# Kernel tuning notes

Hardware: AMD Instinct MI355X
Metric: run time of the kernel (lower is better)

The kernel has to match this reference:

```python
import jax, jax.numpy as jnp
import numpy as np

B, S, T = 4, 512, 512
V, D, F, H, DK, N = 32000, 512, 2048, 8, 64, 6
PAD = 0

# sinusoidal positional encoding table, matching the torch source exactly
_pos = np.arange(max(S, T))[:, None]
_i = np.arange(D // 2)[None, :]
_ang = _pos / (10000.0 ** (2 * _i / D))
_pe = np.empty((max(S, T), D), dtype=np.float32)
_pe[:, 0::2] = np.sin(_ang)
_pe[:, 1::2] = np.cos(_ang)
PE = jnp.asarray(_pe)


def setup_inputs() -> dict:
    key = jax.random.key(0)
    ks = iter(jax.random.split(key, 64))
    s = 0.02
    w = lambda shape: jax.random.normal(next(ks), shape, jnp.float32) * s
    inp = {
        'src': jax.random.randint(next(ks), (B, S), 0, V, jnp.int32),
        'trg': jax.random.randint(next(ks), (B, T), 0, V, jnp.int32),
        'emb_src': w((V, D)).at[PAD].set(0.0),
        'emb_trg': w((V, D)).at[PAD].set(0.0),
        # encoder stacks (leading axis = layer)
        'enc_wq': w((N, D, H * DK)), 'enc_wk': w((N, D, H * DK)),
        'enc_wv': w((N, D, H * DK)), 'enc_wo': w((N, H * DK, D)),
        'enc_ln1_g': jnp.ones((N, D)), 'enc_ln1_b': jnp.zeros((N, D)),
        'enc_w1': w((N, D, F)), 'enc_b1': jnp.zeros((N, F)),
        'enc_w2': w((N, F, D)), 'enc_b2': jnp.zeros((N, D)),
        'enc_ln2_g': jnp.ones((N, D)), 'enc_ln2_b': jnp.zeros((N, D)),
        # decoder stacks
        'dec_wq': w((N, D, H * DK)), 'dec_wk': w((N, D, H * DK)),
        'dec_wv': w((N, D, H * DK)), 'dec_wo': w((N, H * DK, D)),
        'dec_ln1_g': jnp.ones((N, D)), 'dec_ln1_b': jnp.zeros((N, D)),
        'dec_cq': w((N, D, H * DK)), 'dec_ck': w((N, D, H * DK)),
        'dec_cv': w((N, D, H * DK)), 'dec_co': w((N, H * DK, D)),
        'dec_ln2_g': jnp.ones((N, D)), 'dec_ln2_b': jnp.zeros((N, D)),
        'dec_w1': w((N, D, F)), 'dec_b1': jnp.zeros((N, F)),
        'dec_w2': w((N, F, D)), 'dec_b2': jnp.zeros((N, D)),
        'dec_ln3_g': jnp.ones((N, D)), 'dec_ln3_b': jnp.zeros((N, D)),
        'proj': w((D, V)),
    }
    return inp


def _ln(x, g, b, eps=1e-5):
    m = x.mean(-1, keepdims=True)
    v = ((x - m) ** 2).mean(-1, keepdims=True)
    return (x - m) * jax.lax.rsqrt(v + eps) * g + b


def _mha(xq, xkv, wq, wk, wv, wo, mask):
    b, lq, _ = xq.shape
    lk = xkv.shape[1]
    q = (xq @ wq).reshape(b, lq, H, DK).transpose(0, 2, 1, 3)   # bhqd
    k = (xkv @ wk).reshape(b, lk, H, DK).transpose(0, 2, 1, 3)  # bhkd
    v = (xkv @ wv).reshape(b, lk, H, DK).transpose(0, 2, 1, 3)  # bhkd
    scores = jnp.einsum('bhqd,bhkd->bhqk', q, k)
    scores = jnp.where(mask, -jnp.inf, scores)
    attn = jax.nn.softmax(scores * (DK ** -0.5), axis=-1)
    out = jnp.einsum('bhqk,bhkd->bhqd', attn, v)
    out = out.transpose(0, 2, 1, 3).reshape(b, lq, H * DK)
    return out @ wo


def _ffn(x, w1, b1, w2, b2):
    return jax.nn.relu(x @ w1 + b1) @ w2 + b2


def reference(src, trg, emb_src, emb_trg,
              enc_wq, enc_wk, enc_wv, enc_wo, enc_ln1_g, enc_ln1_b,
              enc_w1, enc_b1, enc_w2, enc_b2, enc_ln2_g, enc_ln2_b,
              dec_wq, dec_wk, dec_wv, dec_wo, dec_ln1_g, dec_ln1_b,
              dec_cq, dec_ck, dec_cv, dec_co, dec_ln2_g, dec_ln2_b,
              dec_w1, dec_b1, dec_w2, dec_b2, dec_ln3_g, dec_ln3_b,
              proj):
    scale = D ** 0.5
    src_pad = (src == PAD)[:, None, None, :]                 # [B,1,1,S]
    trg_pad = (trg == PAD)[:, None, None, :]                 # [B,1,1,T]
    causal = jnp.triu(jnp.ones((T, T), bool), 1)[None, None]  # [1,1,T,T]
    trg_mask = trg_pad | causal

    # encoder (dropout = identity in eval)
    x = emb_src[src] * scale + PE[None, :S]

    def enc_step(h, p):
        wq, wk, wv, wo, g1, b1, w1, bb1, w2, bb2, g2, b2 = p
        h = _ln(h + _mha(h, h, wq, wk, wv, wo, src_pad), g1, b1)
        h = _ln(h + _ffn(h, w1, bb1, w2, bb2), g2, b2)
        return h, None

    x_enc, _ = jax.lax.scan(enc_step, x,
        (enc_wq, enc_wk, enc_wv, enc_wo, enc_ln1_g, enc_ln1_b,
         enc_w1, enc_b1, enc_w2, enc_b2, enc_ln2_g, enc_ln2_b))

    # decoder
    y = emb_trg[trg] * scale + PE[None, :T]

    def dec_step(h, p):
        (wq, wk, wv, wo, g1, b1, cq, ck, cv, co, g2, b2,
         w1, bb1, w2, bb2, g3, b3) = p
        h = _ln(h + _mha(h, h, wq, wk, wv, wo, trg_mask), g1, b1)
        h = _ln(h + _mha(h, x_enc, cq, ck, cv, co, src_pad), g2, b2)
        h = _ln(h + _ffn(h, w1, bb1, w2, bb2), g3, b3)
        return h, None

    y, _ = jax.lax.scan(dec_step, y,
        (dec_wq, dec_wk, dec_wv, dec_wo, dec_ln1_g, dec_ln1_b,
         dec_cq, dec_ck, dec_cv, dec_co, dec_ln2_g, dec_ln2_b,
         dec_w1, dec_b1, dec_w2, dec_b2, dec_ln3_g, dec_ln3_b))

    return y @ proj  # [B, T, trg_vocab]
```

## Files before the change

kernel.cpp:

```cpp
#include <hip/hip_runtime.h>
#include <math.h>

#define BBATCH 4
#define SS 512
#define DDIM 512
#define FFN 2048
#define NHEAD 8
#define DHEAD 64
#define NL 6
#define NVOC 32000
#define MTOK (BBATCH*SS)
#define PAD_ID 0
#define MSZE ((size_t)MTOK * DDIM)

typedef unsigned short u16;
typedef __attribute__((ext_vector_type(8))) short short8;
typedef __attribute__((ext_vector_type(4))) float f32x4;

__device__ __forceinline__ u16 f2bf(float f) {
    union { float f; unsigned u; } v; v.f = f;
    unsigned r = ((v.u >> 16) & 1u) + 0x7fffu;
    return (u16)((v.u + r) >> 16);
}

__device__ __forceinline__ void gload16(const u16* g, u16* l) {
    __builtin_amdgcn_global_load_lds(
        (const __attribute__((address_space(1))) void*)g,
        (__attribute__((address_space(3))) void*)l, 16, 0, 0);
}

template<int N> __device__ __forceinline__ void waitv() {
    if constexpr (N == 0)      asm volatile("s_waitcnt vmcnt(0)" ::: "memory");
    else if constexpr (N == 2) asm volatile("s_waitcnt vmcnt(2)" ::: "memory");
    else if constexpr (N == 3) asm volatile("s_waitcnt vmcnt(3)" ::: "memory");
    else if constexpr (N == 4) asm volatile("s_waitcnt vmcnt(4)" ::: "memory");
    else if constexpr (N == 6) asm volatile("s_waitcnt vmcnt(6)" ::: "memory");
    else if constexpr (N == 8) asm volatile("s_waitcnt vmcnt(8)" ::: "memory");
    __builtin_amdgcn_sched_barrier(0);
}
__device__ __forceinline__ void rawbar() {
    __builtin_amdgcn_s_barrier();
    __builtin_amdgcn_sched_barrier(0);
}

template<int BM, int BN, int OUTBF, int RELU, int BIAS>
__device__ __forceinline__ void gemm_core(
    u16* __restrict__ AsB, u16* __restrict__ BsB,
    const u16* __restrict__ A, int lda,
    const u16* __restrict__ B, int ldb,
    void* __restrict__ Cv, int ldc,
    int row0, int col0, int K, const float* __restrict__ bias)
{
    const int tid  = threadIdx.x;
    const int lane = tid & 63;
    const int wid  = tid >> 6;
    const int wr   = wid >> 1, wc = wid & 1;
    constexpr int MF = BM / 32, NF = BN / 32, RA = BM / 64, RB = BN / 64;
    constexpr int LPT = RA + RB;

    const u16* aSrc[RA]; int aOff[RA];
    #pragma unroll
    for (int r = 0; r < RA; r++) {
        int row = (tid >> 2) + r * 64;
        int slot = ((tid & 3) << 4) ^ ((row & 3) << 4);
        aSrc[r] = A + (size_t)(row0 + row) * lda + (slot >> 1);
        aOff[r] = r * 2048 + tid * 8;
    }
    const u16* bSrc[RB]; int bOff[RB];
    #pragma unroll
    for (int r = 0; r < RB; r++) {
        int row = (tid >> 2) + r * 64;
        int slot = ((tid & 3) << 4) ^ ((row & 3) << 4);
        bSrc[r] = B + (size_t)(col0 + row) * ldb + (slot >> 1);
        bOff[r] = r * 2048 + tid * 8;
    }

    f32x4 acc[MF][NF];
    const f32x4 zero = {0.f, 0.f, 0.f, 0.f};
    #pragma unroll
    for (int m = 0; m < MF; m++)
        #pragma unroll
        for (int n = 0; n < NF; n++) acc[m][n] = zero;

    auto issue = [&](int t) {
        u16* ad = AsB + (t & 3) * (BM * 32);
        u16* bd = BsB + (t & 3) * (BN * 32);
        #pragma unroll
        for (int r = 0; r < RA; r++) gload16(aSrc[r] + t * 32, ad + aOff[r]);
        #pragma unroll
        for (int r = 0; r < RB; r++) gload16(bSrc[r] + t * 32, bd + bOff[r]);
    };
    auto comp = [&](int t) {
        const u16* as = AsB + (t & 3) * (BM * 32);
        const u16* bs = BsB + (t & 3) * (BN * 32);
        short8 af[MF], bf[NF];
        #pragma unroll
        for (int m = 0; m < MF; m++) {
            int row = wr * (BM / 2) + m * 16 + (lane & 15);
            int slot = ((lane >> 4) << 4) ^ ((row & 3) << 4);
            af[m] = *(const short8*)&as[row * 32 + (slot >> 1)];
        }
        #pragma unroll
        for (int n = 0; n < NF; n++) {
            int row = wc * (BN / 2) + n * 16 + (lane & 15);
            int slot = ((lane >> 4) << 4) ^ ((row & 3) << 4);
            bf[n] = *(const short8*)&bs[row * 32 + (slot >> 1)];
        }
        __builtin_amdgcn_s_setprio(1);
        #pragma unroll
        for (int m = 0; m < MF; m++)
            #pragma unroll
            for (int n = 0; n < NF; n++)
                acc[m][n] = __builtin_amdgcn_mfma_f32_16x16x32_bf16(af[m], bf[n], acc[m][n], 0, 0, 0);
        __builtin_amdgcn_s_setprio(0);
    };

    const int nt = K / 32;
    issue(0); issue(1); issue(2);
    int t = 0;
    for (; t < nt - 2; ++t) {
        waitv<2 * LPT>();
        rawbar();
        if (t + 3 < nt) issue(t + 3);
        comp(t);
    }
    waitv<LPT>(); rawbar(); comp(nt - 2);
    waitv<0>();   rawbar(); comp(nt - 1);

    const int crow = row0 + wr * (BM / 2);
    const int ccol = col0 + wc * (BN / 2);
    #pragma unroll
    for (int m = 0; m < MF; m++) {
        #pragma unroll
        for (int n = 0; n < NF; n++) {
            int col = ccol + n * 16 + (lane & 15);
            float bv = BIAS ? bias[col] : 0.0f;
            #pragma unroll
            for (int i = 0; i < 4; i++) {
                int row = crow + m * 16 + ((lane >> 4) << 2) + i;
                float v = acc[m][n][i] + bv;
                if (RELU) v = fmaxf(v, 0.0f);
                if (OUTBF) ((u16*)Cv)[(size_t)row * ldc + col] = f2bf(v);
                else       ((float*)Cv)[(size_t)row * ldc + col] = v;
            }
        }
    }
}

template<int BM, int BN, int OUTBF, int RELU, int BIAS, int SWZ = 0>
__global__ __launch_bounds__(256) void mgemm(
    const u16* __restrict__ A, int lda, size_t aSb, size_t aSh,
    const u16* __restrict__ B, int ldb, size_t bSb, size_t bSh,
    void* __restrict__ Cv, int ldc, size_t cSb, size_t cSh,
    int K, const float* __restrict__ bias)
{
    __shared__ __align__(16) u16 As[4 * BM * 32];
    __shared__ __align__(16) u16 Bs[4 * BN * 32];
    int bx = blockIdx.x, by = blockIdx.y;
    if (SWZ) {
        int nwg = gridDim.x * gridDim.y;
        int lin = by * gridDim.x + bx;
        int cpx = nwg >> 3;
        int s = (lin & 7) * cpx + (lin >> 3);
        bx = s % gridDim.x; by = s / gridDim.x;
    }
    const int zb = blockIdx.z >> 3, zh = blockIdx.z & 7;
    const u16* Ab = A + (size_t)zb * aSb + (size_t)zh * aSh;
    const u16* Bb = B + (size_t)zb * bSb + (size_t)zh * bSh;
    void* Cb = OUTBF ? (void*)((u16*)Cv + (size_t)zb * cSb + (size_t)zh * cSh)
                     : (void*)((float*)Cv + (size_t)zb * cSb + (size_t)zh * cSh);
    gemm_core<BM, BN, OUTBF, RELU, BIAS>(As, Bs, Ab, lda, Bb, ldb, Cb, ldc,
                                          by * BM, bx * BN, K, bias);
}

template<int BM, int BN>
__global__ __launch_bounds__(256) void mgemm_dual(
    const u16* __restrict__ A1, int lda1, const u16* __restrict__ B1, int ldb1,
    u16* __restrict__ C1, int ldc1, int nx1, int nblk1,
    const u16* __restrict__ A2, int lda2, const u16* __restrict__ B2, int ldb2,
    u16* __restrict__ C2, int ldc2, int nx2,
    int K)
{
    __shared__ __align__(16) u16 As[4 * BM * 32];
    __shared__ __align__(16) u16 Bs[4 * BN * 32];
    int id = blockIdx.x;
    if (id < nblk1) {
        gemm_core<BM, BN, 1, 0, 0>(As, Bs, A1, lda1, B1, ldb1, C1, ldc1,
                                    (id / nx1) * BM, (id % nx1) * BN, K, nullptr);
    } else {
        id -= nblk1;
        gemm_core<BM, BN, 1, 0, 0>(As, Bs, A2, lda2, B2, ldb2, C2, ldc2,
                                    (id / nx2) * BM, (id % nx2) * BN, K, nullptr);
    }
}

template<int CAUSAL>
__global__ __launch_bounds__(512) void flash_attn(
    const u16* __restrict__ Qp, int ldq,
    const u16* __restrict__ Kp, int ldk,
    const u16* __restrict__ Vtp,
    u16* __restrict__ O,
    const int* __restrict__ ids)
{
    __shared__ __align__(16) u16 Kl[3][64 * 64];
    __shared__ __align__(16) u16 Vl[3][64 * 64];
    __shared__ __align__(16) u16 Pl[8][16 * 64];
    __shared__ float msk[SS];

    const int tid = threadIdx.x, lane = tid & 63, wid = tid >> 6;
    const int bh = blockIdx.y, b = bh >> 3, h = bh & 7;
    const int q0 = blockIdx.x * 128;

    for (int i = tid; i < SS; i += 512)
        msk[i] = (ids[b * SS + i] == PAD_ID) ? -1e30f : 0.0f;

    const int qloc = wid * 16 + (lane & 15);
    const u16* Qb = Qp + (size_t)(b * SS + q0 + qloc) * ldq + h * 64 + ((lane >> 4) * 8);
    short8 qf[2];
    qf[0] = *(const short8*)(Qb);
    qf[1] = *(const short8*)(Qb + 32);

    const u16* Kb = Kp + (size_t)b * SS * ldk + h * 64;
    const u16* Vb = Vtp + (size_t)(h * 64) * MTOK + b * SS;

    auto stage = [&](int buf, int kt) {
        int row = tid >> 3;
        int sl  = tid & 7;
        int ls = sl ^ (row & 7);
        gload16(Kb + (size_t)(kt * 64 + row) * ldk + ls * 8, &Kl[buf][row * 64 + sl * 8]);
        gload16(Vb + (size_t)row * MTOK + kt * 64 + ls * 8, &Vl[buf][row * 64 + sl * 8]);
    };

    const int nt = CAUSAL ? (2 * blockIdx.x + 2) : (SS / 64);

    float m_i[4], l_i[4];
    f32x4 o_acc[4];
    const f32x4 zero = {0.f, 0.f, 0.f, 0.f};
    #pragma unroll
    for (int i = 0; i < 4; i++) { m_i[i] = -1e30f; l_i[i] = 0.0f; }
    #pragma unroll
    for (int n = 0; n < 4; n++) o_acc[n] = zero;

    auto comp = [&](int kt) {
        const int cur = kt % 3;
        f32x4 s_acc[4];
        #pragma unroll
        for (int n = 0; n < 4; n++) s_acc[n] = zero;
        __builtin_amdgcn_s_setprio(1);
        #pragma unroll
        for (int kk = 0; kk < 2; kk++) {
            #pragma unroll
            for (int n = 0; n < 4; n++) {
                int row = n * 16 + (lane & 15);
                int ls = (kk * 4 + (lane >> 4)) ^ (row & 7);
                short8 kf = *(const short8*)&Kl[cur][row * 64 + ls * 8];
                s_acc[n] = __builtin_amdgcn_mfma_f32_16x16x32_bf16(qf[kk], kf, s_acc[n], 0, 0, 0);
            }
        }
        __builtin_amdgcn_s_setprio(0);

        float sv[4][4];
        #pragma unroll
        for (int n = 0; n < 4; n++) {
            int kg = kt * 64 + n * 16 + (lane & 15);
            float mk = msk[kg];
            #pragma unroll
            for (int i = 0; i < 4; i++) {
                float s = s_acc[n][i] * 0.125f + mk;
                if (CAUSAL) {
                    int qg = q0 + wid * 16 + ((lane >> 4) << 2) + i;
                    if (kg > qg) s = -1e30f;
                }
                sv[n][i] = s;
            }
        }
        float pm[4], mn[4], rs[4], ps[4];
        #pragma unroll
        for (int i = 0; i < 4; i++)
            pm[i] = fmaxf(fmaxf(sv[0][i], sv[1][i]), fmaxf(sv[2][i], sv[3][i]));
        #pragma unroll
        for (int i = 0; i < 4; i++) {
            #pragma unroll
            for (int msh = 1; msh <= 8; msh <<= 1)
                pm[i] = fmaxf(pm[i], __shfl_xor(pm[i], msh));
            mn[i] = fmaxf(m_i[i], pm[i]);
            rs[i] = __expf(m_i[i] - mn[i]);
            m_i[i] = mn[i];
        }
        float p[4][4];
        #pragma unroll
        for (int n = 0; n < 4; n++)
            #pragma unroll
            for (int i = 0; i < 4; i++)
                p[n][i] = (sv[n][i] < -1e29f) ? 0.0f : __expf(sv[n][i] - mn[i]);
        #pragma unroll
        for (int i = 0; i < 4; i++) {
            ps[i] = p[0][i] + p[1][i] + p[2][i] + p[3][i];
            #pragma unroll
            for (int msh = 1; msh <= 8; msh <<= 1)
                ps[i] += __shfl_xor(ps[i], msh);
            l_i[i] = l_i[i] * rs[i] + ps[i];
        }
        #pragma unroll
        for (int n = 0; n < 4; n++)
            #pragma unroll
            for (int i = 0; i < 4; i++)
                o_acc[n][i] *= rs[i];

        #pragma unroll
        for (int n = 0; n < 4; n++) {
            int k = n * 16 + (lane & 15);
            #pragma unroll
            for (int i = 0; i < 4; i++) {
                int q = ((lane >> 4) << 2) + i;
                Pl[wid][q * 64 + (((k >> 3) ^ (q & 7)) << 3) + (k & 7)] = f2bf(p[n][i]);
            }
        }
        asm volatile("s_waitcnt lgkmcnt(0)" ::: "memory");
        __builtin_amdgcn_sched_barrier(0);

        __builtin_amdgcn_s_setprio(1);
        #pragma unroll
        for (int kk = 0; kk < 2; kk++) {
            int qrow = lane & 15;
            int lsp = (kk * 4 + (lane >> 4)) ^ (qrow & 7);
            short8 pa = *(const short8*)&Pl[wid][qrow * 64 + lsp * 8];
            #pragma unroll
            for (int nf = 0; nf < 4; nf++) {
                int row = nf * 16 + (lane & 15);
                int vs = (kk * 4 + (lane >> 4)) ^ (row & 7);
                short8 vf = *(const short8*)&Vl[cur][row * 64 + vs * 8];
                o_acc[nf] = __builtin_amdgcn_mfma_f32_16x16x32_bf16(pa, vf, o_acc[nf], 0, 0, 0);
            }
        }
        __builtin_amdgcn_s_setprio(0);
    };

    stage(0, 0);
    stage(1, 1);
    int t = 0;
    for (; t < nt - 1; ++t) {
        waitv<2>();
        rawbar();
        if (t + 2 < nt) stage((t + 2) % 3, t + 2);
        comp(t);
    }
    waitv<0>(); rawbar(); comp(nt - 1);

    #pragma unroll
    for (int nf = 0; nf < 4; nf++) {
        int d = h * 64 + nf * 16 + (lane & 15);
        #pragma unroll
        for (int i = 0; i < 4; i++) {
            int qg = b * SS + q0 + wid * 16 + ((lane >> 4) << 2) + i;
            O[(size_t)qg * DDIM + d] = f2bf(o_acc[nf][i] / l_i[i]);
        }
    }
}

__device__ __forceinline__ void transp_core(const float* __restrict__ src, u16* __restrict__ dst,
                                            int N, int K, int n0, int k0)
{
    __shared__ u16 t[64][65];
    const int tid = threadIdx.x;
    #pragma unroll
    for (int i = 0; i < 16; i++) {
        int idx = tid + i * 256;
        int kr = idx >> 6, nc = idx & 63;
        t[kr][nc] = f2bf(src[(size_t)(k0 + kr) * N + n0 + nc]);
    }
    __syncthreads();
    #pragma unroll
    for (int i = 0; i < 16; i++) {
        int idx = tid + i * 256;
        int nr = idx >> 6, kc = idx & 63;
        dst[(size_t)(n0 + nr) * K + k0 + kc] = t[kc][nr];
    }
}

__global__ __launch_bounds__(256) void transp(const float* __restrict__ src, u16* __restrict__ dst,
                                              int N, int K, size_t sStride, size_t dStride)
{
    transp_core(src + (size_t)blockIdx.z * sStride, dst + (size_t)blockIdx.z * dStride,
                N, K, blockIdx.x * 64, blockIdx.y * 64);
}

#define OFF_QK 0u
#define OFF_WV 524288u
#define OFF_WO 786432u
#define OFF_CQ 1048576u
#define OFF_CK 1310720u
#define OFF_CV 1572864u
#define OFF_CO 1835008u
#define OFF_W1 2097152u
#define OFF_W2 3145728u
#define WBLK   4194304u
#define M2CNT  262144u
#define MF1CNT 1048576u

__global__ __launch_bounds__(256) void transpW(
    const float* p0, const float* p1, const float* p2, const float* p3,
    const float* p4, const float* p5, const float* p6, const float* p7,
    const float* p8, const float* p9, const float* p10, const float* p11,
    u16* __restrict__ wreg)
{
    int z = blockIdx.z;
    int w = z % 12, l = z / 12;
    const float* ptrs[12] = {p0,p1,p2,p3,p4,p5,p6,p7,p8,p9,p10,p11};
    const float* src = ptrs[w] + (size_t)l * M2CNT;
    u16* dst = wreg + (w < 4 ? (size_t)l * WBLK + (size_t)w * M2CNT
                             : (size_t)(NL + l) * WBLK + (size_t)(w - 4) * M2CNT);
    transp_core(src, dst, 512, 512, blockIdx.x * 64, blockIdx.y * 64);
}

__global__ __launch_bounds__(256) void transpF1(const float* __restrict__ e,
                                                const float* __restrict__ d, u16* __restrict__ wreg)
{
    int z = blockIdx.z; int l = z % NL, w = z / NL;
    const float* src = (w ? d : e) + (size_t)l * MF1CNT;
    u16* dst = wreg + (size_t)(w * NL + l) * WBLK + OFF_W1;
    transp_core(src, dst, 2048, 512, blockIdx.x * 64, blockIdx.y * 64);
}

__global__ __launch_bounds__(256) void transpF2(const float* __restrict__ e,
                                                const float* __restrict__ d, u16* __restrict__ wreg)
{
    int z = blockIdx.z; int l = z % NL, w = z / NL;
    const float* src = (w ? d : e) + (size_t)l * MF1CNT;
    u16* dst = wreg + (size_t)(w * NL + l) * WBLK + OFF_W2;
    transp_core(src, dst, 512, 2048, blockIdx.x * 64, blockIdx.y * 64);
}

__global__ void pe_kernel(float* __restrict__ PEt)
{
    int pos = blockIdx.x, d = threadIdx.x;
    int i = d >> 1;
    double freq = exp(-(2.0 * (double)i / (double)DDIM) * log(10000.0));
    double ang = (double)pos * freq;
    PEt[pos * DDIM + d] = (float)((d & 1) ? cos(ang) : sin(ang));
}

__global__ void embed_kernel(const int* __restrict__ src, const int* __restrict__ trg,
                             const float* __restrict__ es, const float* __restrict__ et,
                             const float* __restrict__ PEt,
                             float* __restrict__ X, u16* __restrict__ Xb,
                             float* __restrict__ Y, u16* __restrict__ Ybf)
{
    int gtok = blockIdx.x;
    int d = threadIdx.x;
    bool dec = gtok >= MTOK;
    int tok = dec ? gtok - MTOK : gtok;
    int pos = tok & (SS - 1);
    int id = (dec ? trg : src)[tok];
    const float* emb = dec ? et : es;
    float val = emb[(size_t)id * DDIM + d] * 22.62741699796952f + PEt[pos * DDIM + d];
    (dec ? Y : X)[(size_t)tok * DDIM + d] = val;
    (dec ? Ybf : Xb)[(size_t)tok * DDIM + d] = f2bf(val);
}

__global__ __launch_bounds__(256) void add_ln_kernel(float* __restrict__ x,
    const float* __restrict__ addv, const float* __restrict__ g,
    const float* __restrict__ bta, u16* __restrict__ xb)
{
    int row = blockIdx.x;
    int tid = threadIdx.x;
    size_t base = (size_t)row * DDIM;
    __shared__ float sbuf[4];

    float v0 = x[base + tid]       + addv[base + tid];
    float v1 = x[base + tid + 256] + addv[base + tid + 256];

    float s = v0 + v1;
    #pragma unroll
    for (int o = 32; o > 0; o >>= 1) s += __shfl_down(s, o);
    if ((tid & 63) == 0) sbuf[tid >> 6] = s;
    __syncthreads();
    float mean = (sbuf[0] + sbuf[1] + sbuf[2] + sbuf[3]) * (1.0f / DDIM);
    __syncthreads();

    float d0 = v0 - mean, d1 = v1 - mean;
    float ss = d0 * d0 + d1 * d1;
    #pragma unroll
    for (int o = 32; o > 0; o >>= 1) ss += __shfl_down(ss, o);
    if ((tid & 63) == 0) sbuf[tid >> 6] = ss;
    __syncthreads();
    float var = (sbuf[0] + sbuf[1] + sbuf[2] + sbuf[3]) * (1.0f / DDIM);
    float inv = rsqrtf(var + 1e-5f);

    float o0 = d0 * inv * g[tid]       + bta[tid];
    float o1 = d1 * inv * g[tid + 256] + bta[tid + 256];
    x[base + tid] = o0;
    x[base + tid + 256] = o1;
    xb[base + tid] = f2bf(o0);
    xb[base + tid + 256] = f2bf(o1);
}

__global__ __launch_bounds__(256) void add_ln_red(float* __restrict__ x,
    const float* __restrict__ part, const float* __restrict__ bias,
    const float* __restrict__ g, const float* __restrict__ bta, u16* __restrict__ xb)
{
    int row = blockIdx.x;
    int tid = threadIdx.x;
    size_t base = (size_t)row * DDIM;
    __shared__ float sbuf[4];

    float v0 = x[base + tid]       + bias[tid];
    float v1 = x[base + tid + 256] + bias[tid + 256];
    #pragma unroll
    for (int s4 = 0; s4 < 4; s4++) {
        v0 += part[s4 * MSZE + base + tid];
        v1 += part[s4 * MSZE + base + tid + 256];
    }

    float s = v0 + v1;
    #pragma unroll
    for (int o = 32; o > 0; o >>= 1) s += __shfl_down(s, o);
    if ((tid & 63) == 0) sbuf[tid >> 6] = s;
    __syncthreads();
    float mean = (sbuf[0] + sbuf[1] + sbuf[2] + sbuf[3]) * (1.0f / DDIM);
    __syncthreads();

    float d0 = v0 - mean, d1 = v1 - mean;
    float ss = d0 * d0 + d1 * d1;
    #pragma unroll
    for (int o = 32; o > 0; o >>= 1) ss += __shfl_down(ss, o);
    if ((tid & 63) == 0) sbuf[tid >> 6] = ss;
    __syncthreads();
    float var = (sbuf[0] + sbuf[1] + sbuf[2] + sbuf[3]) * (1.0f / DDIM);
    float inv = rsqrtf(var + 1e-5f);

    float o0 = d0 * inv * g[tid]       + bta[tid];
    float o1 = d1 * inv * g[tid + 256] + bta[tid + 256];
    x[base + tid] = o0;
    x[base + tid + 256] = o1;
    xb[base + tid] = f2bf(o0);
    xb[base + tid + 256] = f2bf(o1);
}

extern "C" void kernel_launch(void* const* d_in, const int* in_sizes, int n_in,
                              void* d_out, int out_size, void* d_ws, size_t ws_size,
                              hipStream_t stream)
{
    (void)in_sizes; (void)n_in; (void)out_size;

    const int*   src      = (const int*)  d_in[0];
    const int*   trg      = (const int*)  d_in[1];
    const float* emb_src  = (const float*)d_in[2];
    const float* emb_trg  = (const float*)d_in[3];
    const float* enc_wq   = (const float*)d_in[4];
    const float* enc_wk   = (const float*)d_in[5];
    const float* enc_wv   = (const float*)d_in[6];
    const float* enc_wo   = (const float*)d_in[7];
    const float* enc_ln1g = (const float*)d_in[8];
    const float* enc_ln1b = (const float*)d_in[9];
    const float* enc_w1   = (const float*)d_in[10];
    const float* enc_b1   = (const float*)d_in[11];
    const float* enc_w2   = (const float*)d_in[12];
    const float* enc_b2   = (const float*)d_in[13];
    const float* enc_ln2g = (const float*)d_in[14];
    const float* enc_ln2b = (const float*)d_in[15];
    const float* dec_wq   = (const float*)d_in[16];
    const float* dec_wk   = (const float*)d_in[17];
    const float* dec_wv   = (const float*)d_in[18];
    const float* dec_wo   = (const float*)d_in[19];
    const float* dec_ln1g = (const float*)d_in[20];
    const float* dec_ln1b = (const float*)d_in[21];
    const float* dec_cq   = (const float*)d_in[22];
    const float* dec_ck   = (const float*)d_in[23];
    const float* dec_cv   = (const float*)d_in[24];
    const float* dec_co   = (const float*)d_in[25];
    const float* dec_ln2g = (const float*)d_in[26];
    const float* dec_ln2b = (const float*)d_in[27];
    const float* dec_w1   = (const float*)d_in[28];
    const float* dec_b1   = (const float*)d_in[29];
    const float* dec_w2   = (const float*)d_in[30];
    const float* dec_b2   = (const float*)d_in[31];
    const float* dec_ln3g = (const float*)d_in[32];
    const float* dec_ln3b = (const float*)d_in[33];
    const float* proj     = (const float*)d_in[34];

    float* OUT = (float*)d_out;
    char* base = (char*)d_ws;

    size_t off = 0;
    auto carve = [&](size_t bytes) { char* p = base + off; off += (bytes + 255) & ~(size_t)255; return p; };

    float* X      = (float*)carve(MSZE * 4);
    float* Yb     = (float*)carve(MSZE * 4);
    float* T1     = (float*)carve(MSZE * 4);
    u16*   Xb     = (u16*)  carve(MSZE * 2);
    u16*   Ybf    = (u16*)  carve(MSZE * 2);
    u16*   QKb    = (u16*)  carve((size_t)MTOK * 1024 * 2);
    u16*   Vt     = (u16*)  carve((size_t)512 * MTOK * 2);
    u16*   CTX    = (u16*)  carve(MSZE * 2);
    u16*   HFF    = (u16*)  carve((size_t)MTOK * FFN * 2);
    u16*   Kcr    = (u16*)  carve((size_t)NL * MTOK * 512 * 2);
    u16*   Vtc    = (u16*)  carve((size_t)NL * 512 * MTOK * 2);
    u16*   projT  = (u16*)  carve((size_t)NVOC * 512 * 2);
    float* PEt    = (float*)carve((size_t)SS * DDIM * 4);
    float* Tp4    = (float*)carve((size_t)4 * MSZE * 4);

    const size_t WFULL_B = (size_t)12 * WBLK * 2;
    bool full = (ws_size >= off + WFULL_B);
    u16* Wreg = (u16*)carve(full ? WFULL_B : (size_t)WBLK * 2);

    auto T = [&](const float* s, u16* d, int Kd, int Nd, size_t ss, size_t ds, int L) {
        transp<<<dim3(Nd / 64, Kd / 64, L), 256, 0, stream>>>(s, d, Nd, Kd, ss, ds);
    };

    pe_kernel<<<SS, DDIM, 0, stream>>>(PEt);
    T(proj, projT, 512, NVOC, 0, 0, 1);
    if (full) {
        transpW<<<dim3(8, 8, 12 * NL), 256, 0, stream>>>(
            enc_wq, enc_wk, enc_wv, enc_wo,
            dec_wq, dec_wk, dec_wv, dec_wo,
            dec_cq, dec_ck, dec_cv, dec_co, Wreg);
        transpF1<<<dim3(32, 8, 2 * NL), 256, 0, stream>>>(enc_w1, dec_w1, Wreg);
        transpF2<<<dim3(8, 32, 2 * NL), 256, 0, stream>>>(enc_w2, dec_w2, Wreg);
    }
    embed_kernel<<<2 * MTOK, DDIM, 0, stream>>>(src, trg, emb_src, emb_trg, PEt, X, Xb, Yb, Ybf);

    auto self_attn = [&](const u16* xsrc, const u16* wb, const int* mask_ids, int causal) {
        mgemm_dual<128, 128><<<dim3(192), 256, 0, stream>>>(
            xsrc, 512, wb + OFF_QK, 512, QKb, 1024, 8, 128,
            wb + OFF_WV, 512, xsrc, 512, Vt, MTOK, 16,
            512);
        if (causal)
            flash_attn<1><<<dim3(4, 32), 512, 0, stream>>>(QKb, 1024, QKb + 512, 1024, Vt, CTX, mask_ids);
        else
            flash_attn<0><<<dim3(4, 32), 512, 0, stream>>>(QKb, 1024, QKb + 512, 1024, Vt, CTX, mask_ids);
        mgemm<64, 64, 0, 0, 0><<<dim3(8, 32, 1), 256, 0, stream>>>(
            CTX, 512, 0, 0, wb + OFF_WO, 512, 0, 0, T1, 512, 0, 0, 512, nullptr);
    };

    auto ffn = [&](const u16* xsrc, const u16* wb, const float* b1) {
        mgemm<128, 128, 1, 1, 1><<<dim3(16, 16, 1), 256, 0, stream>>>(
            xsrc, 512, 0, 0, wb + OFF_W1, 512, 0, 0, HFF, FFN, 0, 0, 512, b1);
        mgemm<128, 128, 0, 0, 0><<<dim3(4, 16, 4), 256, 0, stream>>>(
            HFF, 2048, 0, 512, wb + OFF_W2, 2048, 0, 512,
            Tp4, 512, 0, MSZE, 512, nullptr);
    };

    const size_t M2 = M2CNT, MF1 = MF1CNT;

    for (int l = 0; l < NL; l++) {
        u16* wb;
        if (full) wb = Wreg + (size_t)l * WBLK;
        else {
            wb = Wreg;
            T(enc_wq + l * M2,  wb + OFF_QK,          512, 512,  0, 0, 1);
            T(enc_wk + l * M2,  wb + OFF_QK + M2,     512, 512,  0, 0, 1);
            T(enc_wv + l * M2,  wb + OFF_WV,          512, 512,  0, 0, 1);
            T(enc_wo + l * M2,  wb + OFF_WO,          512, 512,  0, 0, 1);
            T(enc_w1 + l * MF1, wb + OFF_W1,          512, 2048, 0, 0, 1);
            T(enc_w2 + l * MF1, wb + OFF_W2,          2048, 512, 0, 0, 1);
        }
        self_attn(Xb, wb, src, 0);
        add_ln_kernel<<<MTOK, 256, 0, stream>>>(X, T1, enc_ln1g + l * DDIM, enc_ln1b + l * DDIM, Xb);
        ffn(Xb, wb, enc_b1 + l * FFN);
        add_ln_red<<<MTOK, 256, 0, stream>>>(X, Tp4, enc_b2 + l * DDIM,
                                             enc_ln2g + l * DDIM, enc_ln2b + l * DDIM, Xb);
    }

    if (full) {
        u16* Wd = Wreg + (size_t)NL * WBLK;
        mgemm<128, 128, 1, 0, 0><<<dim3(4, 16, NL), 256, 0, stream>>>(
            Xb, 512, 0, 0, Wd + OFF_CK, 512, 0, WBLK, Kcr, 512, 0, (size_t)MTOK * 512, 512, nullptr);
        mgemm<128, 128, 1, 0, 0><<<dim3(16, 4, NL), 256, 0, stream>>>(
            Wd + OFF_CV, 512, 0, WBLK, Xb, 512, 0, 0, Vtc, MTOK, 0, (size_t)512 * MTOK, 512, nullptr);
    }

    for (int l = 0; l < NL; l++) {
        u16* wb;
        if (full) wb = Wreg + (size_t)(NL + l) * WBLK;
        else {
            wb = Wreg;
            T(dec_wq + l * M2,  wb + OFF_QK,          512, 512,  0, 0, 1);
            T(dec_wk + l * M2,  wb + OFF_QK + M2,     512, 512,  0, 0, 1);
            T(dec_wv + l * M2,  wb + OFF_WV,          512, 512,  0, 0, 1);
            T(dec_wo + l * M2,  wb + OFF_WO,          512, 512,  0, 0, 1);
            T(dec_cq + l * M2,  wb + OFF_CQ,          512, 512,  0, 0, 1);
            T(dec_ck + l * M2,  wb + OFF_CK,          512, 512,  0, 0, 1);
            T(dec_cv + l * M2,  wb + OFF_CV,          512, 512,  0, 0, 1);
            T(dec_co + l * M2,  wb + OFF_CO,          512, 512,  0, 0, 1);
            T(dec_w1 + l * MF1, wb + OFF_W1,          512, 2048, 0, 0, 1);
            T(dec_w2 + l * MF1, wb + OFF_W2,          2048, 512, 0, 0, 1);
            mgemm<128, 128, 1, 0, 0><<<dim3(4, 16, 1), 256, 0, stream>>>(
                Xb, 512, 0, 0, wb + OFF_CK, 512, 0, 0, Kcr + (size_t)l * MTOK * 512, 512, 0, 0, 512, nullptr);
            mgemm<128, 128, 1, 0, 0><<<dim3(16, 4, 1), 256, 0, stream>>>(
                wb + OFF_CV, 512, 0, 0, Xb, 512, 0, 0, Vtc + (size_t)l * 512 * MTOK, MTOK, 0, 0, 512, nullptr);
        }
        self_attn(Ybf, wb, trg, 1);
        add_ln_kernel<<<MTOK, 256, 0, stream>>>(Yb, T1, dec_ln1g + l * DDIM, dec_ln1b + l * DDIM, Ybf);
        mgemm<64, 64, 1, 0, 0><<<dim3(8, 32, 1), 256, 0, stream>>>(
            Ybf, 512, 0, 0, wb + OFF_CQ, 512, 0, 0, QKb, 1024, 0, 0, 512, nullptr);
        flash_attn<0><<<dim3(4, 32), 512, 0, stream>>>(
            QKb, 1024, Kcr + (size_t)l * MTOK * 512, 512, Vtc + (size_t)l * 512 * MTOK, CTX, src);
        mgemm<64, 64, 0, 0, 0><<<dim3(8, 32, 1), 256, 0, stream>>>(
            CTX, 512, 0, 0, wb + OFF_CO, 512, 0, 0, T1, 512, 0, 0, 512, nullptr);
        add_ln_kernel<<<MTOK, 256, 0, stream>>>(Yb, T1, dec_ln2g + l * DDIM, dec_ln2b + l * DDIM, Ybf);
        ffn(Ybf, wb, dec_b1 + l * FFN);
        add_ln_red<<<MTOK, 256, 0, stream>>>(Yb, Tp4, dec_b2 + l * DDIM,
                                             dec_ln3g + l * DDIM, dec_ln3b + l * DDIM, Ybf);
    }

    mgemm<128, 128, 0, 0, 0, 1><<<dim3(NVOC / 128, 16, 1), 256, 0, stream>>>(
        Ybf, 512, 0, 0, projT, 512, 0, 0, OUT, NVOC, 0, 0, 512, nullptr);
}
```

Baseline: 1.547 ms.

## Shrink GEMM and attention tiles for more blocks, inline PE into embedding

Flash attention moves from 128-query blocks of 512 threads to 64-query blocks of 256 threads, so each thread stages two K/V rows and the causal tile count changes to match. Most GEMMs, including the QKV dual GEMM, FFN and cross K/V projections, switch from 128x128 to 64x64 tiles to launch more blocks on the many CUs. The positional-encoding table kernel is removed and PE is computed inline in the embedding kernel. Smaller tiles mean less data reuse per block and more global traffic, and the inline PE computes double-precision trig for every element.

```diff
diff --git a/kernel.cpp b/kernel.cpp
--- a/kernel.cpp
+++ b/kernel.cpp
@@ -32,9 +32,7 @@
 template<int N> __device__ __forceinline__ void waitv() {
     if constexpr (N == 0)      asm volatile("s_waitcnt vmcnt(0)" ::: "memory");
     else if constexpr (N == 2) asm volatile("s_waitcnt vmcnt(2)" ::: "memory");
-    else if constexpr (N == 3) asm volatile("s_waitcnt vmcnt(3)" ::: "memory");
     else if constexpr (N == 4) asm volatile("s_waitcnt vmcnt(4)" ::: "memory");
-    else if constexpr (N == 6) asm volatile("s_waitcnt vmcnt(6)" ::: "memory");
     else if constexpr (N == 8) asm volatile("s_waitcnt vmcnt(8)" ::: "memory");
     __builtin_amdgcn_sched_barrier(0);
 }
@@ -195,7 +193,7 @@
 }
 
 template<int CAUSAL>
-__global__ __launch_bounds__(512) void flash_attn(
+__global__ __launch_bounds__(256) void flash_attn(
     const u16* __restrict__ Qp, int ldq,
     const u16* __restrict__ Kp, int ldk,
     const u16* __restrict__ Vtp,
@@ -204,14 +202,15 @@
 {
     __shared__ __align__(16) u16 Kl[3][64 * 64];
     __shared__ __align__(16) u16 Vl[3][64 * 64];
-    __shared__ __align__(16) u16 Pl[8][16 * 64];
+    __shared__ __align__(16) u16 Pl[4][16 * 64];
     __shared__ float msk[SS];
 
     const int tid = threadIdx.x, lane = tid & 63, wid = tid >> 6;
-    const int bh = blockIdx.y, b = bh >> 3, h = bh & 7;
-    const int q0 = blockIdx.x * 128;
-
-    for (int i = tid; i < SS; i += 512)
+    const int qt = blockIdx.x, bh = blockIdx.y;
+    const int b = bh >> 3, h = bh & 7;
+    const int q0 = qt * 64;
+
+    for (int i = tid; i < SS; i += 256)
         msk[i] = (ids[b * SS + i] == PAD_ID) ? -1e30f : 0.0f;
 
     const int qloc = wid * 16 + (lane & 15);
@@ -224,14 +223,17 @@
     const u16* Vb = Vtp + (size_t)(h * 64) * MTOK + b * SS;
 
     auto stage = [&](int buf, int kt) {
-        int row = tid >> 3;
-        int sl  = tid & 7;
-        int ls = sl ^ (row & 7);
-        gload16(Kb + (size_t)(kt * 64 + row) * ldk + ls * 8, &Kl[buf][row * 64 + sl * 8]);
-        gload16(Vb + (size_t)row * MTOK + kt * 64 + ls * 8, &Vl[buf][row * 64 + sl * 8]);
+        int row = tid >> 3, sl = tid & 7;
+        #pragma unroll
+        for (int r = 0; r < 2; r++) {
+            int rr = row + r * 32;
+            int ls = sl ^ (rr & 7);
+            gload16(Kb + (size_t)(kt * 64 + rr) * ldk + ls * 8, &Kl[buf][rr * 64 + sl * 8]);
+            gload16(Vb + (size_t)rr * MTOK + kt * 64 + ls * 8, &Vl[buf][rr * 64 + sl * 8]);
+        }
     };
 
-    const int nt = CAUSAL ? (2 * blockIdx.x + 2) : (SS / 64);
+    const int nt = CAUSAL ? (qt + 1) : (SS / 64);
 
     float m_i[4], l_i[4];
     f32x4 o_acc[4];
@@ -340,7 +342,7 @@
     stage(1, 1);
     int t = 0;
     for (; t < nt - 1; ++t) {
-        waitv<2>();
+        waitv<4>();
         rawbar();
         if (t + 2 < nt) stage((t + 2) % 3, t + 2);
         comp(t);
@@ -431,18 +433,8 @@
     transp_core(src, dst, 512, 2048, blockIdx.x * 64, blockIdx.y * 64);
 }
 
-__global__ void pe_kernel(float* __restrict__ PEt)
-{
-    int pos = blockIdx.x, d = threadIdx.x;
-    int i = d >> 1;
-    double freq = exp(-(2.0 * (double)i / (double)DDIM) * log(10000.0));
-    double ang = (double)pos * freq;
-    PEt[pos * DDIM + d] = (float)((d & 1) ? cos(ang) : sin(ang));
-}
-
 __global__ void embed_kernel(const int* __restrict__ src, const int* __restrict__ trg,
                              const float* __restrict__ es, const float* __restrict__ et,
-                             const float* __restrict__ PEt,
                              float* __restrict__ X, u16* __restrict__ Xb,
                              float* __restrict__ Y, u16* __restrict__ Ybf)
 {
@@ -453,7 +445,11 @@
     int pos = tok & (SS - 1);
     int id = (dec ? trg : src)[tok];
     const float* emb = dec ? et : es;
-    float val = emb[(size_t)id * DDIM + d] * 22.62741699796952f + PEt[pos * DDIM + d];
+    int i = d >> 1;
+    double freq = exp(-(2.0 * (double)i / (double)DDIM) * log(10000.0));
+    double ang = (double)pos * freq;
+    float pe = (float)((d & 1) ? cos(ang) : sin(ang));
+    float val = emb[(size_t)id * DDIM + d] * 22.62741699796952f + pe;
     (dec ? Y : X)[(size_t)tok * DDIM + d] = val;
     (dec ? Ybf : Xb)[(size_t)tok * DDIM + d] = f2bf(val);
 }
@@ -597,7 +593,6 @@
     u16*   Kcr    = (u16*)  carve((size_t)NL * MTOK * 512 * 2);
     u16*   Vtc    = (u16*)  carve((size_t)NL * 512 * MTOK * 2);
     u16*   projT  = (u16*)  carve((size_t)NVOC * 512 * 2);
-    float* PEt    = (float*)carve((size_t)SS * DDIM * 4);
     float* Tp4    = (float*)carve((size_t)4 * MSZE * 4);
 
     const size_t WFULL_B = (size_t)12 * WBLK * 2;
@@ -608,7 +603,6 @@
         transp<<<dim3(Nd / 64, Kd / 64, L), 256, 0, stream>>>(s, d, Nd, Kd, ss, ds);
     };
 
-    pe_kernel<<<SS, DDIM, 0, stream>>>(PEt);
     T(proj, projT, 512, NVOC, 0, 0, 1);
     if (full) {
         transpW<<<dim3(8, 8, 12 * NL), 256, 0, stream>>>(
@@ -618,25 +612,25 @@
         transpF1<<<dim3(32, 8, 2 * NL), 256, 0, stream>>>(enc_w1, dec_w1, Wreg);
         transpF2<<<dim3(8, 32, 2 * NL), 256, 0, stream>>>(enc_w2, dec_w2, Wreg);
     }
-    embed_kernel<<<2 * MTOK, DDIM, 0, stream>>>(src, trg, emb_src, emb_trg, PEt, X, Xb, Yb, Ybf);
+    embed_kernel<<<2 * MTOK, DDIM, 0, stream>>>(src, trg, emb_src, emb_trg, X, Xb, Yb, Ybf);
 
     auto self_attn = [&](const u16* xsrc, const u16* wb, const int* mask_ids, int causal) {
-        mgemm_dual<128, 128><<<dim3(192), 256, 0, stream>>>(
-            xsrc, 512, wb + OFF_QK, 512, QKb, 1024, 8, 128,
-            wb + OFF_WV, 512, xsrc, 512, Vt, MTOK, 16,
+        mgemm_dual<64, 64><<<dim3(768), 256, 0, stream>>>(
+            xsrc, 512, wb + OFF_QK, 512, QKb, 1024, 16, 512,
+            wb + OFF_WV, 512, xsrc, 512, Vt, MTOK, 32,
             512);
         if (causal)
-            flash_attn<1><<<dim3(4, 32), 512, 0, stream>>>(QKb, 1024, QKb + 512, 1024, Vt, CTX, mask_ids);
+            flash_attn<1><<<dim3(8, 32), 256, 0, stream>>>(QKb, 1024, QKb + 512, 1024, Vt, CTX, mask_ids);
         else
-            flash_attn<0><<<dim3(4, 32), 512, 0, stream>>>(QKb, 1024, QKb + 512, 1024, Vt, CTX, mask_ids);
+            flash_attn<0><<<dim3(8, 32), 256, 0, stream>>>(QKb, 1024, QKb + 512, 1024, Vt, CTX, mask_ids);
         mgemm<64, 64, 0, 0, 0><<<dim3(8, 32, 1), 256, 0, stream>>>(
             CTX, 512, 0, 0, wb + OFF_WO, 512, 0, 0, T1, 512, 0, 0, 512, nullptr);
     };
 
     auto ffn = [&](const u16* xsrc, const u16* wb, const float* b1) {
-        mgemm<128, 128, 1, 1, 1><<<dim3(16, 16, 1), 256, 0, stream>>>(
+        mgemm<64, 64, 1, 1, 1><<<dim3(32, 32, 1), 256, 0, stream>>>(
             xsrc, 512, 0, 0, wb + OFF_W1, 512, 0, 0, HFF, FFN, 0, 0, 512, b1);
-        mgemm<128, 128, 0, 0, 0><<<dim3(4, 16, 4), 256, 0, stream>>>(
+        mgemm<64, 64, 0, 0, 0><<<dim3(8, 32, 4), 256, 0, stream>>>(
             HFF, 2048, 0, 512, wb + OFF_W2, 2048, 0, 512,
             Tp4, 512, 0, MSZE, 512, nullptr);
     };
@@ -648,12 +642,12 @@
         if (full) wb = Wreg + (size_t)l * WBLK;
         else {
             wb = Wreg;
-            T(enc_wq + l * M2,  wb + OFF_QK,          512, 512,  0, 0, 1);
-            T(enc_wk + l * M2,  wb + OFF_QK + M2,     512, 512,  0, 0, 1);
-            T(enc_wv + l * M2,  wb + OFF_WV,          512, 512,  0, 0, 1);
-            T(enc_wo + l * M2,  wb + OFF_WO,          512, 512,  0, 0, 1);
-            T(enc_w1 + l * MF1, wb + OFF_W1,          512, 2048, 0, 0, 1);
-            T(enc_w2 + l * MF1, wb + OFF_W2,          2048, 512, 0, 0, 1);
+            T(enc_wq + l * M2,  wb + OFF_QK,      512, 512,  0, 0, 1);
+            T(enc_wk + l * M2,  wb + OFF_QK + M2, 512, 512,  0, 0, 1);
+            T(enc_wv + l * M2,  wb + OFF_WV,      512, 512,  0, 0, 1);
+            T(enc_wo + l * M2,  wb + OFF_WO,      512, 512,  0, 0, 1);
+            T(enc_w1 + l * MF1, wb + OFF_W1,      512, 2048, 0, 0, 1);
+            T(enc_w2 + l * MF1, wb + OFF_W2,      2048, 512, 0, 0, 1);
         }
         self_attn(Xb, wb, src, 0);
         add_ln_kernel<<<MTOK, 256, 0, stream>>>(X, T1, enc_ln1g + l * DDIM, enc_ln1b + l * DDIM, Xb);
@@ -664,9 +658,9 @@
 
     if (full) {
         u16* Wd = Wreg + (size_t)NL * WBLK;
-        mgemm<128, 128, 1, 0, 0><<<dim3(4, 16, NL), 256, 0, stream>>>(
+        mgemm<64, 64, 1, 0, 0><<<dim3(8, 32, NL), 256, 0, stream>>>(
             Xb, 512, 0, 0, Wd + OFF_CK, 512, 0, WBLK, Kcr, 512, 0, (size_t)MTOK * 512, 512, nullptr);
-        mgemm<128, 128, 1, 0, 0><<<dim3(16, 4, NL), 256, 0, stream>>>(
+        mgemm<64, 64, 1, 0, 0><<<dim3(32, 8, NL), 256, 0, stream>>>(
             Wd + OFF_CV, 512, 0, WBLK, Xb, 512, 0, 0, Vtc, MTOK, 0, (size_t)512 * MTOK, 512, nullptr);
     }
 
@@ -675,26 +669,26 @@
         if (full) wb = Wreg + (size_t)(NL + l) * WBLK;
         else {
             wb = Wreg;
-            T(dec_wq + l * M2,  wb + OFF_QK,          512, 512,  0, 0, 1);
-            T(dec_wk + l * M2,  wb + OFF_QK + M2,     512, 512,  0, 0, 1);
-            T(dec_wv + l * M2,  wb + OFF_WV,          512, 512,  0, 0, 1);
-            T(dec_wo + l * M2,  wb + OFF_WO,          512, 512,  0, 0, 1);
-            T(dec_cq + l * M2,  wb + OFF_CQ,          512, 512,  0, 0, 1);
-            T(dec_ck + l * M2,  wb + OFF_CK,          512, 512,  0, 0, 1);
-            T(dec_cv + l * M2,  wb + OFF_CV,          512, 512,  0, 0, 1);
-            T(dec_co + l * M2,  wb + OFF_CO,          512, 512,  0, 0, 1);
-            T(dec_w1 + l * MF1, wb + OFF_W1,          512, 2048, 0, 0, 1);
-            T(dec_w2 + l * MF1, wb + OFF_W2,          2048, 512, 0, 0, 1);
-            mgemm<128, 128, 1, 0, 0><<<dim3(4, 16, 1), 256, 0, stream>>>(
+            T(dec_wq + l * M2,  wb + OFF_QK,      512, 512,  0, 0, 1);
+            T(dec_wk + l * M2,  wb + OFF_QK + M2, 512, 512,  0, 0, 1);
+            T(dec_wv + l * M2,  wb + OFF_WV,      512, 512,  0, 0, 1);
+            T(dec_wo + l * M2,  wb + OFF_WO,      512, 512,  0, 0, 1);
+            T(dec_cq + l * M2,  wb + OFF_CQ,      512, 512,  0, 0, 1);
+            T(dec_ck + l * M2,  wb + OFF_CK,      512, 512,  0, 0, 1);
+            T(dec_cv + l * M2,  wb + OFF_CV,      512, 512,  0, 0, 1);
+            T(dec_co + l * M2,  wb + OFF_CO,      512, 512,  0, 0, 1);
+            T(dec_w1 + l * MF1, wb + OFF_W1,      512, 2048, 0, 0, 1);
+            T(dec_w2 + l * MF1, wb + OFF_W2,      2048, 512, 0, 0, 1);
+            mgemm<64, 64, 1, 0, 0><<<dim3(8, 32, 1), 256, 0, stream>>>(
                 Xb, 512, 0, 0, wb + OFF_CK, 512, 0, 0, Kcr + (size_t)l * MTOK * 512, 512, 0, 0, 512, nullptr);
-            mgemm<128, 128, 1, 0, 0><<<dim3(16, 4, 1), 256, 0, stream>>>(
+            mgemm<64, 64, 1, 0, 0><<<dim3(32, 8, 1), 256, 0, stream>>>(
                 wb + OFF_CV, 512, 0, 0, Xb, 512, 0, 0, Vtc + (size_t)l * 512 * MTOK, MTOK, 0, 0, 512, nullptr);
         }
         self_attn(Ybf, wb, trg, 1);
         add_ln_kernel<<<MTOK, 256, 0, stream>>>(Yb, T1, dec_ln1g + l * DDIM, dec_ln1b + l * DDIM, Ybf);
         mgemm<64, 64, 1, 0, 0><<<dim3(8, 32, 1), 256, 0, stream>>>(
             Ybf, 512, 0, 0, wb + OFF_CQ, 512, 0, 0, QKb, 1024, 0, 0, 512, nullptr);
-        flash_attn<0><<<dim3(4, 32), 512, 0, stream>>>(
+        flash_attn<0><<<dim3(8, 32), 256, 0, stream>>>(
             QKb, 1024, Kcr + (size_t)l * MTOK * 512, 512, Vtc + (size_t)l * 512 * MTOK, CTX, src);
         mgemm<64, 64, 0, 0, 0><<<dim3(8, 32, 1), 256, 0, stream>>>(
             CTX, 512, 0, 0, wb + OFF_CO, 512, 0, 0, T1, 512, 0, 0, 512, nullptr);
```

Measured after the change: 1.473 ms. 1.05x faster.
